# Performance work log

Hardware: AMD Instinct MI355X
Metric: run time of the kernel (lower is better)

## Reference

```python
import jax, jax.numpy as jnp
import numpy as np

B, S, D, E = 4, 4096, 2048, 8


def setup_inputs() -> dict:
    key = jax.random.key(0)
    kx, kw, kb = jax.random.split(key, 3)
    x = jax.random.normal(kx, (B, S, D), dtype=jnp.float32)
    # nn.Linear(d_model, n_experts): weight [E, D], bias [E]
    bound = 1.0 / np.sqrt(D)
    W = jax.random.uniform(kw, (E, D), minval=-bound, maxval=bound, dtype=jnp.float32)
    b = jax.random.uniform(kb, (E,), minval=-bound, maxval=bound, dtype=jnp.float32)
    return {"x": x, "W": W, "b": b}


def reference(x, W, b):
    # logits = x @ W^T + b : [B, S, E]
    logits = jnp.einsum("bsd,ed->bse", x, W) + b
    gate = jax.nn.softmax(logits, axis=-1)
    top2_val, top2_idx = jax.lax.top_k(gate, 2)  # [B, S, 2] each
    return (top2_val, top2_idx, gate)
```

## Files before the change

### kernel.cpp

```cpp
#include <hip/hip_runtime.h>
#include <hip/hip_bf16.h>
#include <math.h>


#define NTOK   16384
#define DM     2048
#define NE     8

__device__ __forceinline__ float fold4(const float4 a) {
    return (a.x + a.y) + (a.z + a.w);
}

__device__ __forceinline__ float reduce_scatter8(const float4* acc, const int j) {
    float v0 = fold4(acc[0]), v1 = fold4(acc[1]), v2 = fold4(acc[2]), v3 = fold4(acc[3]);
    float v4 = fold4(acc[4]), v5 = fold4(acc[5]), v6 = fold4(acc[6]), v7 = fold4(acc[7]);
    float s0 = v0 + __shfl_xor(v0, 1, 8);
    float s1 = v1 + __shfl_xor(v1, 1, 8);
    float s2 = v2 + __shfl_xor(v2, 1, 8);
    float s3 = v3 + __shfl_xor(v3, 1, 8);
    float s4 = v4 + __shfl_xor(v4, 1, 8);
    float s5 = v5 + __shfl_xor(v5, 1, 8);
    float s6 = v6 + __shfl_xor(v6, 1, 8);
    float s7 = v7 + __shfl_xor(v7, 1, 8);
    const bool b0 = (j & 1);
    float t0 = b0 ? s1 : s0;
    float t1 = b0 ? s3 : s2;
    float t2 = b0 ? s5 : s4;
    float t3 = b0 ? s7 : s6;
    float p0 = t0 + __shfl_xor(t0, 2, 8);
    float p1 = t1 + __shfl_xor(t1, 2, 8);
    float p2 = t2 + __shfl_xor(t2, 2, 8);
    float p3 = t3 + __shfl_xor(t3, 2, 8);
    const bool b1 = (j & 2);
    float u0 = b1 ? p1 : p0;
    float u1 = b1 ? p3 : p2;
    float q0 = u0 + __shfl_xor(u0, 4, 8);
    float q1 = u1 + __shfl_xor(u1, 4, 8);
    return (j & 4) ? q1 : q0;
}

__device__ __forceinline__ void softmax_top2(const float logit, const int j,
                                             const int token, float* __restrict__ out) {
    float m = logit;
#pragma unroll
    for (int s = 4; s; s >>= 1) m = fmaxf(m, __shfl_xor(m, s, 8));
    const float ex = expf(logit - m);
    float sum = ex;
#pragma unroll
    for (int s = 4; s; s >>= 1) sum += __shfl_xor(sum, s, 8);
    const float gate = ex / sum;

    out[65536 + token * NE + j] = gate;

    float g1 = gate; int e1 = j;
#pragma unroll
    for (int s = 4; s; s >>= 1) {
        const float og = __shfl_xor(g1, s, 8);
        const int   oe = __shfl_xor(e1, s, 8);
        if (og > g1 || (og == g1 && oe < e1)) { g1 = og; e1 = oe; }
    }
    float g2 = (j == e1) ? -INFINITY : gate; int e2 = j;
#pragma unroll
    for (int s = 4; s; s >>= 1) {
        const float og = __shfl_xor(g2, s, 8);
        const int   oe = __shfl_xor(e2, s, 8);
        if (og > g2 || (og == g2 && oe < e2)) { g2 = og; e2 = oe; }
    }
    if (j == 0) {
        out[token * 2 + 0]         = g1;
        out[token * 2 + 1]         = g2;
        out[32768 + token * 2 + 0] = (float)e1;
        out[32768 + token * 2 + 1] = (float)e2;
    }
}

__global__ __launch_bounds__(256, 1) void top2router_kernel(
    const float* __restrict__ x,
    const float* __restrict__ W,
    const float* __restrict__ b,
    float* __restrict__ out)
{
    __shared__ __align__(16) float sW[NE * DM];

    const int t = threadIdx.x;

    {
        const float4* __restrict__ Wv = reinterpret_cast<const float4*>(W);
        float4* sWv = reinterpret_cast<float4*>(sW);
#pragma unroll
        for (int i = 0; i < 16; ++i)
            sWv[i * 256 + t] = Wv[i * 256 + t];
    }
    __syncthreads();

    const int lane = t & 63;
    const int wave = t >> 6;
    const int j    = lane & 7;
    const int st   = lane >> 3;
    const int base = (blockIdx.x * 4 + wave) * 16;
    const int tok0 = base + st;
    const int tok1 = base + st + 8;

    const float* __restrict__ xp0 = x + (size_t)tok0 * DM + (j << 2);
    const float* __restrict__ xp1 = x + (size_t)tok1 * DM + (j << 2);
    const float bj = b[j];

    float4 acc0[NE], acc1[NE];
#pragma unroll
    for (int e = 0; e < NE; ++e) {
        acc0[e] = make_float4(0.f, 0.f, 0.f, 0.f);
        acc1[e] = make_float4(0.f, 0.f, 0.f, 0.f);
    }

    float4 xa0 = *reinterpret_cast<const float4*>(xp0);
    float4 xa1 = *reinterpret_cast<const float4*>(xp1);

#pragma unroll 3
    for (int k = 0; k < 63; ++k) {
        const float4 xb0 = *reinterpret_cast<const float4*>(xp0 + ((k + 1) << 5));
        const float4 xb1 = *reinterpret_cast<const float4*>(xp1 + ((k + 1) << 5));
        const float* wbase = &sW[(k << 5) + (j << 2)];
#pragma unroll
        for (int e = 0; e < NE; ++e) {
            const float4 wv = *reinterpret_cast<const float4*>(wbase + e * DM);
            acc0[e].x = fmaf(xa0.x, wv.x, acc0[e].x);
            acc0[e].y = fmaf(xa0.y, wv.y, acc0[e].y);
            acc0[e].z = fmaf(xa0.z, wv.z, acc0[e].z);
            acc0[e].w = fmaf(xa0.w, wv.w, acc0[e].w);
            acc1[e].x = fmaf(xa1.x, wv.x, acc1[e].x);
            acc1[e].y = fmaf(xa1.y, wv.y, acc1[e].y);
            acc1[e].z = fmaf(xa1.z, wv.z, acc1[e].z);
            acc1[e].w = fmaf(xa1.w, wv.w, acc1[e].w);
        }
        xa0 = xb0;
        xa1 = xb1;
    }
    {
        const float* wbase = &sW[(63 << 5) + (j << 2)];
#pragma unroll
        for (int e = 0; e < NE; ++e) {
            const float4 wv = *reinterpret_cast<const float4*>(wbase + e * DM);
            acc0[e].x = fmaf(xa0.x, wv.x, acc0[e].x);
            acc0[e].y = fmaf(xa0.y, wv.y, acc0[e].y);
            acc0[e].z = fmaf(xa0.z, wv.z, acc0[e].z);
            acc0[e].w = fmaf(xa0.w, wv.w, acc0[e].w);
            acc1[e].x = fmaf(xa1.x, wv.x, acc1[e].x);
            acc1[e].y = fmaf(xa1.y, wv.y, acc1[e].y);
            acc1[e].z = fmaf(xa1.z, wv.z, acc1[e].z);
            acc1[e].w = fmaf(xa1.w, wv.w, acc1[e].w);
        }
    }

    const float logit0 = reduce_scatter8(acc0, j) + bj;
    const float logit1 = reduce_scatter8(acc1, j) + bj;

    softmax_top2(logit0, j, tok0, out);
    softmax_top2(logit1, j, tok1, out);
}

extern "C" void kernel_launch(void* const* d_in, const int* in_sizes, int n_in,
                              void* d_out, int out_size, void* d_ws, size_t ws_size,
                              hipStream_t stream) {
    const float* x = (const float*)d_in[0];
    const float* W = (const float*)d_in[1];
    const float* b = (const float*)d_in[2];
    float* out = (float*)d_out;

    top2router_kernel<<<256, 256, 0, stream>>>(x, W, b, out);
}
```

Measured before the change: 195.1 us.

## Split reduction dimension across waves with per-wave W slice and LDS combine

Each block now handles 16 tokens, and its four waves each cover a quarter of the model dimension. Every wave stages only its own 512-column slice of W in shared memory, without a block-wide barrier before compute. The launch grows from 256 to 1024 blocks, with launch bounds allowing two blocks per CU, and x is read with nontemporal loads. Partial logits are summed through shared memory after one barrier, and two waves then do softmax/top-2. This is meant to raise parallelism and memory-level concurrency in the bandwidth-bound x stream, at the cost of reloading W per block and an extra LDS reduction step.

New measurement: 183.7 us. -5.8%, faster.

```diff
diff --git a/kernel.cpp b/kernel.cpp
--- a/kernel.cpp
+++ b/kernel.cpp
@@ -3,9 +3,13 @@
 #include <math.h>
 
 
-#define NTOK   16384
-#define DM     2048
-#define NE     8
+#define NTOK  16384
+#define DM    2048
+#define NE    8
+#define TPB   16
+#define KQ    512
+
+typedef float v4f __attribute__((ext_vector_type(4)));
 
 __device__ __forceinline__ float fold4(const float4 a) {
     return (a.x + a.y) + (a.z + a.w);
@@ -74,36 +78,38 @@
     }
 }
 
-__global__ __launch_bounds__(256, 1) void top2router_kernel(
+__global__ __launch_bounds__(256, 2) void router_fused(
     const float* __restrict__ x,
     const float* __restrict__ W,
     const float* __restrict__ b,
     float* __restrict__ out)
 {
-    __shared__ __align__(16) float sW[NE * DM];
+    __shared__ __align__(16) float sWq[4 * NE * KQ];
+    __shared__ float sPart[4 * TPB * NE];
 
-    const int t = threadIdx.x;
+    const int t    = threadIdx.x;
+    const int wv   = t >> 6;
+    const int lane = t & 63;
+    const int j    = lane & 7;
+    const int st   = lane >> 3;
 
     {
         const float4* __restrict__ Wv = reinterpret_cast<const float4*>(W);
-        float4* sWv = reinterpret_cast<float4*>(sW);
+        float4* sWv = reinterpret_cast<float4*>(&sWq[wv * NE * KQ]);
 #pragma unroll
-        for (int i = 0; i < 16; ++i)
-            sWv[i * 256 + t] = Wv[i * 256 + t];
+        for (int i = 0; i < 16; ++i) {
+            const int L  = i * 64 + lane;
+            const int e  = L >> 7;
+            const int f4 = L & 127;
+            sWv[L] = Wv[e * (DM / 4) + wv * (KQ / 4) + f4];
+        }
     }
-    __syncthreads();
 
-    const int lane = t & 63;
-    const int wave = t >> 6;
-    const int j    = lane & 7;
-    const int st   = lane >> 3;
-    const int base = (blockIdx.x * 4 + wave) * 16;
-    const int tok0 = base + st;
-    const int tok1 = base + st + 8;
-
-    const float* __restrict__ xp0 = x + (size_t)tok0 * DM + (j << 2);
-    const float* __restrict__ xp1 = x + (size_t)tok1 * DM + (j << 2);
-    const float bj = b[j];
+    const int tokbase = blockIdx.x * TPB;
+    const int tok0 = tokbase + st;
+    const int tok1 = tokbase + st + 8;
+    const float* __restrict__ xp0 = x + (size_t)tok0 * DM + wv * KQ + (j << 2);
+    const float* __restrict__ xp1 = x + (size_t)tok1 * DM + wv * KQ + (j << 2);
 
     float4 acc0[NE], acc1[NE];
 #pragma unroll
@@ -112,50 +118,50 @@
         acc1[e] = make_float4(0.f, 0.f, 0.f, 0.f);
     }
 
-    float4 xa0 = *reinterpret_cast<const float4*>(xp0);
-    float4 xa1 = *reinterpret_cast<const float4*>(xp1);
-
-#pragma unroll 3
-    for (int k = 0; k < 63; ++k) {
-        const float4 xb0 = *reinterpret_cast<const float4*>(xp0 + ((k + 1) << 5));
-        const float4 xb1 = *reinterpret_cast<const float4*>(xp1 + ((k + 1) << 5));
-        const float* wbase = &sW[(k << 5) + (j << 2)];
+    v4f xa0 = __builtin_nontemporal_load(reinterpret_cast<const v4f*>(xp0));
+    v4f xa1 = __builtin_nontemporal_load(reinterpret_cast<const v4f*>(xp1));
+#pragma unroll
+    for (int it = 0; it < 16; ++it) {
+        v4f xn0, xn1;
+        if (it < 15) {
+            xn0 = __builtin_nontemporal_load(
+                reinterpret_cast<const v4f*>(xp0 + ((it + 1) << 5)));
+            xn1 = __builtin_nontemporal_load(
+                reinterpret_cast<const v4f*>(xp1 + ((it + 1) << 5)));
+        }
+        const float* wbase = &sWq[wv * NE * KQ + (it << 5) + (j << 2)];
 #pragma unroll
         for (int e = 0; e < NE; ++e) {
-            const float4 wv = *reinterpret_cast<const float4*>(wbase + e * DM);
-            acc0[e].x = fmaf(xa0.x, wv.x, acc0[e].x);
-            acc0[e].y = fmaf(xa0.y, wv.y, acc0[e].y);
-            acc0[e].z = fmaf(xa0.z, wv.z, acc0[e].z);
-            acc0[e].w = fmaf(xa0.w, wv.w, acc0[e].w);
-            acc1[e].x = fmaf(xa1.x, wv.x, acc1[e].x);
-            acc1[e].y = fmaf(xa1.y, wv.y, acc1[e].y);
-            acc1[e].z = fmaf(xa1.z, wv.z, acc1[e].z);
-            acc1[e].w = fmaf(xa1.w, wv.w, acc1[e].w);
+            const float4 wvv = *reinterpret_cast<const float4*>(wbase + e * KQ);
+            acc0[e].x = fmaf(xa0.x, wvv.x, acc0[e].x);
+            acc0[e].y = fmaf(xa0.y, wvv.y, acc0[e].y);
+            acc0[e].z = fmaf(xa0.z, wvv.z, acc0[e].z);
+            acc0[e].w = fmaf(xa0.w, wvv.w, acc0[e].w);
+            acc1[e].x = fmaf(xa1.x, wvv.x, acc1[e].x);
+            acc1[e].y = fmaf(xa1.y, wvv.y, acc1[e].y);
+            acc1[e].z = fmaf(xa1.z, wvv.z, acc1[e].z);
+            acc1[e].w = fmaf(xa1.w, wvv.w, acc1[e].w);
         }
-        xa0 = xb0;
-        xa1 = xb1;
-    }
-    {
-        const float* wbase = &sW[(63 << 5) + (j << 2)];
-#pragma unroll
-        for (int e = 0; e < NE; ++e) {
-            const float4 wv = *reinterpret_cast<const float4*>(wbase + e * DM);
-            acc0[e].x = fmaf(xa0.x, wv.x, acc0[e].x);
-            acc0[e].y = fmaf(xa0.y, wv.y, acc0[e].y);
-            acc0[e].z = fmaf(xa0.z, wv.z, acc0[e].z);
-            acc0[e].w = fmaf(xa0.w, wv.w, acc0[e].w);
-            acc1[e].x = fmaf(xa1.x, wv.x, acc1[e].x);
-            acc1[e].y = fmaf(xa1.y, wv.y, acc1[e].y);
-            acc1[e].z = fmaf(xa1.z, wv.z, acc1[e].z);
-            acc1[e].w = fmaf(xa1.w, wv.w, acc1[e].w);
-        }
+        xa0 = xn0;
+        xa1 = xn1;
     }
 
-    const float logit0 = reduce_scatter8(acc0, j) + bj;
-    const float logit1 = reduce_scatter8(acc1, j) + bj;
+    const float p0 = reduce_scatter8(acc0, j);
+    const float p1 = reduce_scatter8(acc1, j);
+    sPart[wv * (TPB * NE) + st * NE + j]       = p0;
+    sPart[wv * (TPB * NE) + (st + 8) * NE + j] = p1;
+    __syncthreads();
 
-    softmax_top2(logit0, j, tok0, out);
-    softmax_top2(logit1, j, tok1, out);
+    if (wv < 2) {
+        const int tk   = wv * 8 + st;
+        const int gtok = tokbase + tk;
+        float s = sPart[0 * (TPB * NE) + tk * NE + j]
+                + sPart[1 * (TPB * NE) + tk * NE + j]
+                + sPart[2 * (TPB * NE) + tk * NE + j]
+                + sPart[3 * (TPB * NE) + tk * NE + j];
+        const float logit = s + b[j];
+        softmax_top2(logit, j, gtok, out);
+    }
 }
 
 extern "C" void kernel_launch(void* const* d_in, const int* in_sizes, int n_in,
@@ -166,5 +172,5 @@
     const float* b = (const float*)d_in[2];
     float* out = (float*)d_out;
 
-    top2router_kernel<<<256, 256, 0, stream>>>(x, W, b, out);
+    router_fused<<<NTOK / TPB, 256, 0, stream>>>(x, W, b, out);
 }
```
